# Optimization experiments

Hardware: AMD Instinct MI355X
Metric: run time of the kernel (lower is better)

## Reference

```python
import jax, jax.numpy as jnp
import numpy as np

N_HEAD = 16


def setup_inputs() -> dict:
    key = jax.random.key(0)
    ks = jax.random.split(key, 9)
    B, T, C = 4, 2048, 1024
    s = 1.0 / np.sqrt(C)
    x = jax.random.normal(ks[0], (B, T, C), dtype=jnp.float32)
    Wq = jax.random.normal(ks[1], (C, C), dtype=jnp.float32) * s
    bq = jax.random.normal(ks[2], (C,), dtype=jnp.float32) * 0.01
    Wk = jax.random.normal(ks[3], (C, C), dtype=jnp.float32) * s
    bk = jax.random.normal(ks[4], (C,), dtype=jnp.float32) * 0.01
    Wv = jax.random.normal(ks[5], (C, C), dtype=jnp.float32) * s
    bv = jax.random.normal(ks[6], (C,), dtype=jnp.float32) * 0.01
    Wp = jax.random.normal(ks[7], (C, C), dtype=jnp.float32) * s
    bp = jax.random.normal(ks[8], (C,), dtype=jnp.float32) * 0.01
    return {"x": x, "Wq": Wq, "bq": bq, "Wk": Wk, "bk": bk,
            "Wv": Wv, "bv": bv, "Wp": Wp, "bp": bp}


def reference(x, Wq, bq, Wk, bk, Wv, bv, Wp, bp):
    B, T, C = x.shape
    H = N_HEAD
    d = C // H
    # projections (torch Linear: x @ W.T + b)
    q = (x @ Wq.T + bq).reshape(B, T, H, d)  # [B,T,H,d]
    k = (x @ Wk.T + bk).reshape(B, T, H, d)
    v = (x @ Wv.T + bv).reshape(B, T, H, d)
    scale = 1.0 / jnp.sqrt(jnp.asarray(d, dtype=x.dtype))
    # scores: [B,H,T,T]
    att = jnp.einsum('bqhd,bkhd->bhqk', q, k) * scale
    causal = jnp.tril(jnp.ones((T, T), dtype=bool))  # [T,T]
    att = jnp.where(causal[None, None], att, jnp.asarray(-jnp.inf, dtype=att.dtype))
    att = jax.nn.softmax(att, axis=-1)
    y = jnp.einsum('bhqk,bkhd->bqhd', att, v).reshape(B, T, C)
    return y @ Wp.T + bp
```

## Files before the change

### kernel.cpp

```cpp
#include <hip/hip_runtime.h>
#include <hip/hip_bf16.h>

typedef __attribute__((ext_vector_type(8))) short bf16x8;
typedef __attribute__((ext_vector_type(4))) float f32x4;

static constexpr int Tt = 2048;
static constexpr int Cc = 1024;
static constexpr int Dd = 64;
static constexpr int Mm = 8192;

static constexpr size_t XN = (size_t)Mm * Cc;
static constexpr size_t WN = (size_t)Cc * Cc;

__device__ __forceinline__ void async_copy16(void* lds, const void* g) {
  __builtin_amdgcn_global_load_lds(
      (const __attribute__((address_space(1))) void*)g,
      (__attribute__((address_space(3))) void*)lds, 16, 0, 0);
}

__device__ __forceinline__ unsigned short f2bf(float f) {
  union { float f; unsigned int u; } v; v.f = f;
  unsigned int r = (v.u + 0x7fffu + ((v.u >> 16) & 1u)) >> 16;
  return (unsigned short)r;
}
__device__ __forceinline__ unsigned int pack2bf(float f0, float f1) {
  unsigned int b0 = __float_as_uint(f0) + 0x8000u;
  unsigned int b1 = __float_as_uint(f1) + 0x8000u;
  return (b1 & 0xffff0000u) | (b0 >> 16);
}
__device__ __forceinline__ unsigned int cvtpk2bf(float f0, float f1) {
  unsigned int r;
  asm("v_cvt_pk_bf16_f32 %0, %1, %2" : "=v"(r) : "v"(f0), "v"(f1));
  return r;
}
__device__ __forceinline__ uint4 ldconv_f32(const float* p) {
  float4 lo = *(const float4*)p;
  float4 hi = *(const float4*)(p + 4);
  uint4 r;
  r.x = pack2bf(lo.x, lo.y);
  r.y = pack2bf(lo.z, lo.w);
  r.z = pack2bf(hi.x, hi.y);
  r.w = pack2bf(hi.z, hi.w);
  return r;
}

__global__ __launch_bounds__(256) void convert_all(
    const float* __restrict__ x, const float* __restrict__ wq,
    const float* __restrict__ wk, const float* __restrict__ wv,
    unsigned short* __restrict__ dst,
    const float* __restrict__ wp, unsigned short* __restrict__ wpb)
{
  if (blockIdx.x >= 5632) {
    const size_t i = ((size_t)(blockIdx.x - 5632) * 256 + threadIdx.x) * 8;
    *(uint4*)(wpb + i) = ldconv_f32(wp + i);
    return;
  }
  const size_t i = ((size_t)blockIdx.x * 256 + threadIdx.x) * 8;
  const float* s; size_t off;
  if (i < XN)                { s = x;  off = 0; }
  else if (i < XN + WN)      { s = wq; off = XN; }
  else if (i < XN + 2 * WN)  { s = wk; off = XN + WN; }
  else                       { s = wv; off = XN + 2 * WN; }
  *(uint4*)(dst + i) = ldconv_f32(s + (i - off));
}

template <int MODE>
__device__ __forceinline__ void gemm_async_body(
    unsigned short* As, unsigned short* Bs,
    const unsigned short* __restrict__ A,
    const unsigned short* __restrict__ Bt,
    const float* __restrict__ bias,
    unsigned short* __restrict__ out, float mult)
{
  const int tid  = threadIdx.x;
  const int wave = tid >> 6;
  const int lane = tid & 63;
  const int m16  = lane & 15;
  const int quad = lane >> 4;
  const int row0 = blockIdx.x * 128;
  const int col0 = blockIdx.y * 128;
  const int wm = (wave >> 1) * 64;
  const int wn = (wave & 1) * 64;

  f32x4 acc[4][4] = {};

  const unsigned short* Ag[4];
  const unsigned short* Bg[4];
#pragma unroll
  for (int j = 0; j < 4; ++j) {
    const int c  = j * 256 + tid;
    const int rw = c >> 3;
    const int sw = (c & 7) ^ (rw & 7);
    Ag[j] = A  + (size_t)(row0 + rw) * Cc + sw * 8;
    Bg[j] = Bt + (size_t)(col0 + rw) * Cc + sw * 8;
  }

  for (int k0 = 0; k0 < Cc; k0 += 64) {
    __syncthreads();
#pragma unroll
    for (int j = 0; j < 4; ++j)
      async_copy16((char*)As + j * 4096 + wave * 1024, Ag[j] + k0);
#pragma unroll
    for (int j = 0; j < 4; ++j)
      async_copy16((char*)Bs + j * 4096 + wave * 1024, Bg[j] + k0);
    __syncthreads();
#pragma unroll
    for (int kk = 0; kk < 2; ++kk) {
      const int chp = (kk * 4 + quad) ^ (m16 & 7);
      bf16x8 af[4], bfr[4];
#pragma unroll
      for (int i = 0; i < 4; ++i)
        af[i] = *(const bf16x8*)(As + (wm + i * 16 + m16) * 64 + chp * 8);
#pragma unroll
      for (int j = 0; j < 4; ++j)
        bfr[j] = *(const bf16x8*)(Bs + (wn + j * 16 + m16) * 64 + chp * 8);
#pragma unroll
      for (int i = 0; i < 4; ++i)
#pragma unroll
        for (int j = 0; j < 4; ++j)
          acc[i][j] = __builtin_amdgcn_mfma_f32_16x16x32_bf16(af[i], bfr[j], acc[i][j], 0, 0, 0);
    }
  }

  float bvj[4];
#pragma unroll
  for (int j = 0; j < 4; ++j)
    bvj[j] = bias[col0 + wn + j * 16 + m16];
#pragma unroll
  for (int i = 0; i < 4; ++i) {
    const int rbase = row0 + wm + i * 16 + quad * 4;
#pragma unroll
    for (int j = 0; j < 4; ++j) {
      const int col = col0 + wn + j * 16 + m16;
      const float bv = bvj[j];
      if (MODE == 0) {
#pragma unroll
        for (int r = 0; r < 4; ++r)
          out[(size_t)(rbase + r) * Cc + col] = f2bf((acc[i][j][r] + bv) * mult);
      } else if (MODE == 1) {
        const int t0 = rbase & (Tt - 1);
        const int b  = rbase >> 11;
        ushort4 pk;
        pk.x = f2bf(acc[i][j][0] + bv);
        pk.y = f2bf(acc[i][j][1] + bv);
        pk.z = f2bf(acc[i][j][2] + bv);
        pk.w = f2bf(acc[i][j][3] + bv);
        *(ushort4*)(out + (size_t)(b * Cc + col) * Tt + t0) = pk;
      } else {
        float* outf = (float*)out;
#pragma unroll
        for (int r = 0; r < 4; ++r)
          outf[(size_t)(rbase + r) * Cc + col] = acc[i][j][r] + bv;
      }
    }
  }
}

__global__ __launch_bounds__(256) void qkv_gemm(
    const unsigned short* __restrict__ Xb,
    const unsigned short* __restrict__ Wqb, const float* __restrict__ bq,
    const unsigned short* __restrict__ Wkb, const float* __restrict__ bk,
    const unsigned short* __restrict__ Wvb, const float* __restrict__ bv,
    unsigned short* Qw, unsigned short* Kw, unsigned short* Vtw)
{
  __shared__ __align__(16) unsigned short smem[16384];
  const int z = blockIdx.z;
  if (z == 0)      gemm_async_body<0>(smem, smem + 8192, Xb, Wqb, bq, Qw, 0.125f * 1.44269504f);
  else if (z == 1) gemm_async_body<0>(smem, smem + 8192, Xb, Wkb, bk, Kw, 1.0f);
  else             gemm_async_body<1>(smem, smem + 8192, Xb, Wvb, bv, Vtw, 1.0f);
}

__global__ __launch_bounds__(256) void proj_gemm_pre(
    const unsigned short* __restrict__ Yb,
    const unsigned short* __restrict__ Wpb, const float* __restrict__ bp,
    float* __restrict__ out)
{
  __shared__ __align__(16) unsigned short smem[16384];
  gemm_async_body<2>(smem, smem + 8192, Yb, Wpb, bp, (unsigned short*)out, 1.0f);
}

__global__ __launch_bounds__(256) void attn_strip16(
    const unsigned short* __restrict__ Q,
    const unsigned short* __restrict__ Kg,
    const unsigned short* __restrict__ Vt,
    unsigned short* __restrict__ Y)
{
  __shared__ __align__(16) unsigned short KV[2 * 8192];

  const int tid  = threadIdx.x;
  const int wave = tid >> 6;
  const int lane = tid & 63;
  const int m16  = lane & 15;
  const int quad = lane >> 4;

  const int bh = blockIdx.x;
  const int p  = blockIdx.y;
  const int b = bh >> 4, h = bh & 15;

  const unsigned short* Kb = Kg + (size_t)(b * Tt) * Cc + h * Dd;
  const unsigned short* Vb = Vt + (size_t)(b * Cc + h * Dd) * Tt;

  const int maxH = 32 - p;
  const int TOT  = 33;
  const int chp  = quad ^ ((m16 >> 1) & 3);

  bf16x8 onesA;
#pragma unroll
  for (int i = 0; i < 8; ++i) onesA[i] = (short)0x3F80;

  const unsigned short* pK[2];
  const unsigned short* pV[2];
#pragma unroll
  for (int ii = 0; ii < 2; ++ii) {
    const int cc  = ii * 256 + tid;
    const int kkS = cc >> 8;
    const int rrS = (cc >> 2) & 63;
    const int chd = (cc & 3) ^ ((rrS >> 1) & 3);
    pK[ii] = Kb + (size_t)rrS * Cc + kkS * 32 + chd * 8;
    pV[ii] = Vb + (size_t)rrS * Tt + kkS * 32 + chd * 8;
  }
  const unsigned short* pK0[2] = {pK[0], pK[1]};
  const unsigned short* pV0[2] = {pV[0], pV[1]};

  int qw = (127 - 4 * p - wave) * 16;
  bf16x8 qf[2];
  {
    const unsigned short* Qb = Q + (size_t)(b * Tt + qw + m16) * Cc + h * Dd;
#pragma unroll
    for (int kk = 0; kk < 2; ++kk)
      qf[kk] = *(const bf16x8*)(Qb + kk * 32 + quad * 8);
  }
  f32x4 o[4] = {};
  f32x4 lz = {};

  auto writeout = [&](int qw_) {
    const float l = lz[0];
    const float inv = (l > 0.f) ? (1.0f / l) : 0.f;
    unsigned short* yp = Y + (size_t)(b * Tt + qw_ + m16) * Cc + h * Dd + quad * 4;
#pragma unroll
    for (int jn = 0; jn < 4; ++jn) {
      uint2 pk;
      pk.x = cvtpk2bf(o[jn][0] * inv, o[jn][1] * inv);
      pk.y = cvtpk2bf(o[jn][2] * inv, o[jn][3] * inv);
      *(uint2*)(yp + jn * 16) = pk;
    }
  };

  {
    char* KbufB = (char*)KV;
    char* VbufB = KbufB + 8192;
#pragma unroll
    for (int ii = 0; ii < 2; ++ii) {
      async_copy16(KbufB + ii * 4096 + wave * 1024, pK[ii]);
      async_copy16(VbufB + ii * 4096 + wave * 1024, pV[ii]);
    }
#pragma unroll
    for (int ii = 0; ii < 2; ++ii) { pK[ii] += 64 * Cc; pV[ii] += 64; }
  }

  for (int g = 0; g < TOT; ++g) {
    if (g == maxH) {
      writeout(qw);
      qw = (4 * p + wave) * 16;
      const unsigned short* Qb = Q + (size_t)(b * Tt + qw + m16) * Cc + h * Dd;
#pragma unroll
      for (int kk = 0; kk < 2; ++kk)
        qf[kk] = *(const bf16x8*)(Qb + kk * 32 + quad * 8);
#pragma unroll
      for (int jn = 0; jn < 4; ++jn)
        o[jn] = f32x4{0.f, 0.f, 0.f, 0.f};
      lz = f32x4{0.f, 0.f, 0.f, 0.f};
    }
    const int kt  = (g < maxH) ? g : g - maxH;
    const int k0  = kt * 64;
    const int buf = g & 1;

    __syncthreads();
    if (g + 1 < TOT) {
      if (g + 1 == maxH) {
#pragma unroll
        for (int ii = 0; ii < 2; ++ii) { pK[ii] = pK0[ii]; pV[ii] = pV0[ii]; }
      }
      char* KbufB = (char*)KV + (buf ^ 1) * 16384;
      char* VbufB = KbufB + 8192;
#pragma unroll
      for (int ii = 0; ii < 2; ++ii) {
        async_copy16(KbufB + ii * 4096 + wave * 1024, pK[ii]);
        async_copy16(VbufB + ii * 4096 + wave * 1024, pV[ii]);
      }
#pragma unroll
      for (int ii = 0; ii < 2; ++ii) { pK[ii] += 64 * Cc; pV[ii] += 64; }
    }

    const unsigned short* Kbuf = KV + buf * 8192;
    const unsigned short* Vbuf = Kbuf + 4096;
    bf16x8 kf[2][4], vf[2][4];
#pragma unroll
    for (int kk = 0; kk < 2; ++kk)
#pragma unroll
      for (int jn = 0; jn < 4; ++jn) {
        kf[kk][jn] = *(const bf16x8*)(Kbuf + kk * 2048 + (jn * 16 + m16) * 32 + chp * 8);
        vf[kk][jn] = *(const bf16x8*)(Vbuf + kk * 2048 + (jn * 16 + m16) * 32 + chp * 8);
      }

    const int smin = qw;
    f32x4 sv[4] = {};
    __builtin_amdgcn_s_setprio(1);
#pragma unroll
    for (int kk = 0; kk < 2; ++kk)
#pragma unroll
      for (int jn = 0; jn < 4; ++jn)
        sv[jn] = __builtin_amdgcn_mfma_f32_16x16x32_bf16(kf[kk][jn], qf[kk], sv[jn], 0, 0, 0);
    __builtin_amdgcn_s_setprio(0);

    if (k0 + 63 <= smin) {
#pragma unroll
      for (int jn = 0; jn < 4; ++jn)
#pragma unroll
        for (int r = 0; r < 4; ++r)
          sv[jn][r] = __builtin_exp2f(sv[jn][r]);
    } else {
      const int qcol = smin + m16;
#pragma unroll
      for (int jn = 0; jn < 4; ++jn)
#pragma unroll
        for (int r = 0; r < 4; ++r)
          sv[jn][r] = (k0 + jn * 16 + quad * 4 + r > qcol)
                          ? 0.f : __builtin_exp2f(sv[jn][r]);
    }

    unsigned int P2[4][2];
#pragma unroll
    for (int jn = 0; jn < 4; ++jn) {
      P2[jn][0] = cvtpk2bf(sv[jn][0], sv[jn][1]);
      P2[jn][1] = cvtpk2bf(sv[jn][2], sv[jn][3]);
    }
#pragma unroll
    for (int kk = 0; kk < 2; ++kk) {
      auto r0 = __builtin_amdgcn_permlane32_swap(P2[2 * kk][0], P2[2 * kk + 1][0], false, false);
      auto t0 = __builtin_amdgcn_permlane16_swap(r0[0], r0[1], false, false);
      auto r1 = __builtin_amdgcn_permlane32_swap(P2[2 * kk][1], P2[2 * kk + 1][1], false, false);
      auto t1 = __builtin_amdgcn_permlane16_swap(r1[0], r1[1], false, false);
      uint4 u;
      u.x = t0[0];
      u.y = t1[0];
      u.z = t0[1];
      u.w = t1[1];
      union { uint4 u4; bf16x8 bf; } cv; cv.u4 = u;
      __builtin_amdgcn_s_setprio(1);
      lz = __builtin_amdgcn_mfma_f32_16x16x32_bf16(onesA, cv.bf, lz, 0, 0, 0);
#pragma unroll
      for (int jn = 0; jn < 4; ++jn)
        o[jn] = __builtin_amdgcn_mfma_f32_16x16x32_bf16(vf[kk][jn], cv.bf, o[jn], 0, 0, 0);
      __builtin_amdgcn_s_setprio(0);
    }
  }

  writeout(qw);
}

__global__ __launch_bounds__(256) void proj_gemm(
    const unsigned short* __restrict__ Y,
    const float* __restrict__ Wp, const float* __restrict__ bp,
    float* __restrict__ out)
{
  __shared__ __align__(16) unsigned short As[8192];
  __shared__ __align__(16) unsigned short Bs[8192];
  const int tid  = threadIdx.x;
  const int wave = tid >> 6;
  const int lane = tid & 63;
  const int m16  = lane & 15;
  const int quad = lane >> 4;
  const int row0 = blockIdx.x * 128;
  const int col0 = blockIdx.y * 128;
  const int wm = (wave >> 1) * 64;
  const int wn = (wave & 1) * 64;
  const int chp = quad ^ ((m16 >> 1) & 3);

  f32x4 acc[4][4] = {};

  const int c0 = tid, c1 = 256 + tid;
  const int sw0 = (c0 & 3) ^ ((c0 >> 3) & 3);
  const int sw1 = (c1 & 3) ^ ((c1 >> 3) & 3);
  const unsigned short* Ag0 = Y + (size_t)(row0 + (c0 >> 2)) * Cc + sw0 * 8;
  const unsigned short* Ag1 = Y + (size_t)(row0 + (c1 >> 2)) * Cc + sw1 * 8;
  const float* Bg0 = Wp + (size_t)(col0 + (c0 >> 2)) * Cc + (c0 & 3) * 8;
  const float* Bg1 = Wp + (size_t)(col0 + (c1 >> 2)) * Cc + (c1 & 3) * 8;
  const int bd0 = ((c0 >> 2) * 4 + sw0) * 8;
  const int bd1 = ((c1 >> 2) * 4 + sw1) * 8;

  uint4 b0 = ldconv_f32(Bg0);
  uint4 b1 = ldconv_f32(Bg1);

  async_copy16((char*)As + wave * 1024,        Ag0);
  async_copy16((char*)As + 4096 + wave * 1024, Ag1);
  *(uint4*)(Bs + bd0) = b0;
  *(uint4*)(Bs + bd1) = b1;
  b0 = ldconv_f32(Bg0 + 32);
  b1 = ldconv_f32(Bg1 + 32);

  int buf = 0;
  for (int k0 = 0; k0 < Cc; k0 += 32) {
    __syncthreads();
    if (k0 + 32 < Cc) {
      char* Ab = (char*)As + (buf ^ 1) * 8192;
      async_copy16(Ab + wave * 1024,        Ag0 + k0 + 32);
      async_copy16(Ab + 4096 + wave * 1024, Ag1 + k0 + 32);
      *(uint4*)(Bs + (buf ^ 1) * 4096 + bd0) = b0;
      *(uint4*)(Bs + (buf ^ 1) * 4096 + bd1) = b1;
      if (k0 + 64 < Cc) {
        b0 = ldconv_f32(Bg0 + k0 + 64);
        b1 = ldconv_f32(Bg1 + k0 + 64);
      }
    }
    const unsigned short* Asb = As + buf * 4096;
    const unsigned short* Bsb = Bs + buf * 4096;
    bf16x8 af[4], bfr[4];
#pragma unroll
    for (int i = 0; i < 4; ++i)
      af[i] = *(const bf16x8*)(Asb + (wm + i * 16 + m16) * 32 + chp * 8);
#pragma unroll
    for (int j = 0; j < 4; ++j)
      bfr[j] = *(const bf16x8*)(Bsb + (wn + j * 16 + m16) * 32 + chp * 8);
#pragma unroll
    for (int i = 0; i < 4; ++i)
#pragma unroll
      for (int j = 0; j < 4; ++j)
        acc[i][j] = __builtin_amdgcn_mfma_f32_16x16x32_bf16(af[i], bfr[j], acc[i][j], 0, 0, 0);
    buf ^= 1;
  }

#pragma unroll
  for (int i = 0; i < 4; ++i) {
    const int rbase = row0 + wm + i * 16 + quad * 4;
#pragma unroll
    for (int j = 0; j < 4; ++j) {
      const int col = col0 + wn + j * 16 + m16;
      const float bv = bp[col];
#pragma unroll
      for (int r = 0; r < 4; ++r)
        out[(size_t)(rbase + r) * Cc + col] = acc[i][j][r] + bv;
    }
  }
}

extern "C" void kernel_launch(void* const* d_in, const int* in_sizes, int n_in,
                              void* d_out, int out_size, void* d_ws, size_t ws_size,
                              hipStream_t stream)
{
  const float* x  = (const float*)d_in[0];
  const float* Wq = (const float*)d_in[1];
  const float* bq = (const float*)d_in[2];
  const float* Wk = (const float*)d_in[3];
  const float* bk = (const float*)d_in[4];
  const float* Wv = (const float*)d_in[5];
  const float* bv = (const float*)d_in[6];
  const float* Wp = (const float*)d_in[7];
  const float* bp = (const float*)d_in[8];

  unsigned short* ws  = (unsigned short*)d_ws;
  unsigned short* Qw  = ws;
  unsigned short* Kw  = ws + (size_t)1 * XN;
  unsigned short* Vtw = ws + (size_t)2 * XN;
  unsigned short* Yw  = ws + (size_t)3 * XN;
  unsigned short* Wpb = ws + (size_t)4 * XN;
  const bool pre = ws_size >= ((size_t)4 * XN + WN) * sizeof(unsigned short);

  unsigned short* cvt = (unsigned short*)d_out;
  unsigned short* Xb  = cvt;
  unsigned short* Wqb = cvt + XN;
  unsigned short* Wkb = cvt + XN + WN;
  unsigned short* Wvb = cvt + XN + 2 * WN;
  float* out = (float*)d_out;

  convert_all<<<pre ? 6144 : 5632, 256, 0, stream>>>(x, Wq, Wk, Wv, cvt, Wp, Wpb);
  qkv_gemm<<<dim3(64, 8, 3), 256, 0, stream>>>(Xb, Wqb, bq, Wkb, bk, Wvb, bv, Qw, Kw, Vtw);
  attn_strip16<<<dim3(64, 16), 256, 0, stream>>>(Qw, Kw, Vtw, Yw);
  if (pre) proj_gemm_pre<<<dim3(64, 8), 256, 0, stream>>>(Yw, Wpb, bp, out);
  else     proj_gemm<<<dim3(64, 8), 256, 0, stream>>>(Yw, Wp, bp, out);
}
```

Baseline: 254.9 us.

## Fuse high and low query strips into one KV pass per block

The attention kernel now gives each wave four 16-row query strips: two from the high half and two from the low half. A single sweep over the KV tiles serves all four strips, and low strips skip tiles past their causal limit. Before, each wave handled one strip at a time and reloaded the K/V tiles for its second pass. Each staged K/V tile now feeds more MFMA work, and the grid is halved, which lowers parallelism and raises register use for the extra accumulators.

```diff
diff --git a/kernel.cpp b/kernel.cpp
--- a/kernel.cpp
+++ b/kernel.cpp
@@ -179,7 +179,7 @@
   gemm_async_body<2>(smem, smem + 8192, Yb, Wpb, bp, (unsigned short*)out, 1.0f);
 }
 
-__global__ __launch_bounds__(256) void attn_strip16(
+__global__ __launch_bounds__(256) void attn_fused(
     const unsigned short* __restrict__ Q,
     const unsigned short* __restrict__ Kg,
     const unsigned short* __restrict__ Vt,
@@ -200,9 +200,8 @@
   const unsigned short* Kb = Kg + (size_t)(b * Tt) * Cc + h * Dd;
   const unsigned short* Vb = Vt + (size_t)(b * Cc + h * Dd) * Tt;
 
-  const int maxH = 32 - p;
-  const int TOT  = 33;
-  const int chp  = quad ^ ((m16 >> 1) & 3);
+  const int TOT = 32 - 2 * p;
+  const int chp = quad ^ ((m16 >> 1) & 3);
 
   bf16x8 onesA;
 #pragma unroll
@@ -219,32 +218,21 @@
     pK[ii] = Kb + (size_t)rrS * Cc + kkS * 32 + chd * 8;
     pV[ii] = Vb + (size_t)rrS * Tt + kkS * 32 + chd * 8;
   }
-  const unsigned short* pK0[2] = {pK[0], pK[1]};
-  const unsigned short* pV0[2] = {pV[0], pV[1]};
-
-  int qw = (127 - 4 * p - wave) * 16;
-  bf16x8 qf[2];
-  {
-    const unsigned short* Qb = Q + (size_t)(b * Tt + qw + m16) * Cc + h * Dd;
+
+  const int qH = (63 - 4 * p - wave) * 32;
+  const int qL = (4 * p + wave) * 32;
+  int qrow[4] = {qH, qH + 16, qL, qL + 16};
+
+  bf16x8 qf[4][2];
+#pragma unroll
+  for (int u = 0; u < 4; ++u) {
+    const unsigned short* Qb = Q + (size_t)(b * Tt + qrow[u] + m16) * Cc + h * Dd;
 #pragma unroll
     for (int kk = 0; kk < 2; ++kk)
-      qf[kk] = *(const bf16x8*)(Qb + kk * 32 + quad * 8);
-  }
-  f32x4 o[4] = {};
-  f32x4 lz = {};
-
-  auto writeout = [&](int qw_) {
-    const float l = lz[0];
-    const float inv = (l > 0.f) ? (1.0f / l) : 0.f;
-    unsigned short* yp = Y + (size_t)(b * Tt + qw_ + m16) * Cc + h * Dd + quad * 4;
-#pragma unroll
-    for (int jn = 0; jn < 4; ++jn) {
-      uint2 pk;
-      pk.x = cvtpk2bf(o[jn][0] * inv, o[jn][1] * inv);
-      pk.y = cvtpk2bf(o[jn][2] * inv, o[jn][3] * inv);
-      *(uint2*)(yp + jn * 16) = pk;
-    }
-  };
+      qf[u][kk] = *(const bf16x8*)(Qb + kk * 32 + quad * 8);
+  }
+  f32x4 o[4][4] = {};
+  f32x4 lz[4] = {};
 
   {
     char* KbufB = (char*)KV;
@@ -259,28 +247,11 @@
   }
 
   for (int g = 0; g < TOT; ++g) {
-    if (g == maxH) {
-      writeout(qw);
-      qw = (4 * p + wave) * 16;
-      const unsigned short* Qb = Q + (size_t)(b * Tt + qw + m16) * Cc + h * Dd;
-#pragma unroll
-      for (int kk = 0; kk < 2; ++kk)
-        qf[kk] = *(const bf16x8*)(Qb + kk * 32 + quad * 8);
-#pragma unroll
-      for (int jn = 0; jn < 4; ++jn)
-        o[jn] = f32x4{0.f, 0.f, 0.f, 0.f};
-      lz = f32x4{0.f, 0.f, 0.f, 0.f};
-    }
-    const int kt  = (g < maxH) ? g : g - maxH;
-    const int k0  = kt * 64;
+    const int k0  = g * 64;
     const int buf = g & 1;
 
     __syncthreads();
     if (g + 1 < TOT) {
-      if (g + 1 == maxH) {
-#pragma unroll
-        for (int ii = 0; ii < 2; ++ii) { pK[ii] = pK0[ii]; pV[ii] = pV0[ii]; }
-      }
       char* KbufB = (char*)KV + (buf ^ 1) * 16384;
       char* VbufB = KbufB + 8192;
 #pragma unroll
@@ -303,60 +274,76 @@
         vf[kk][jn] = *(const bf16x8*)(Vbuf + kk * 2048 + (jn * 16 + m16) * 32 + chp * 8);
       }
 
-    const int smin = qw;
-    f32x4 sv[4] = {};
-    __builtin_amdgcn_s_setprio(1);
-#pragma unroll
-    for (int kk = 0; kk < 2; ++kk)
-#pragma unroll
-      for (int jn = 0; jn < 4; ++jn)
-        sv[jn] = __builtin_amdgcn_mfma_f32_16x16x32_bf16(kf[kk][jn], qf[kk], sv[jn], 0, 0, 0);
-    __builtin_amdgcn_s_setprio(0);
-
-    if (k0 + 63 <= smin) {
-#pragma unroll
-      for (int jn = 0; jn < 4; ++jn)
-#pragma unroll
-        for (int r = 0; r < 4; ++r)
-          sv[jn][r] = __builtin_exp2f(sv[jn][r]);
-    } else {
-      const int qcol = smin + m16;
-#pragma unroll
-      for (int jn = 0; jn < 4; ++jn)
-#pragma unroll
-        for (int r = 0; r < 4; ++r)
-          sv[jn][r] = (k0 + jn * 16 + quad * 4 + r > qcol)
-                          ? 0.f : __builtin_exp2f(sv[jn][r]);
-    }
-
-    unsigned int P2[4][2];
+#pragma unroll
+    for (int u = 0; u < 4; ++u) {
+      const int smin = qrow[u];
+      if (k0 > smin + 15) continue;
+      f32x4 sv[4] = {};
+      __builtin_amdgcn_s_setprio(1);
+#pragma unroll
+      for (int kk = 0; kk < 2; ++kk)
+#pragma unroll
+        for (int jn = 0; jn < 4; ++jn)
+          sv[jn] = __builtin_amdgcn_mfma_f32_16x16x32_bf16(kf[kk][jn], qf[u][kk], sv[jn], 0, 0, 0);
+      __builtin_amdgcn_s_setprio(0);
+
+      if (k0 + 63 <= smin) {
+#pragma unroll
+        for (int jn = 0; jn < 4; ++jn)
+#pragma unroll
+          for (int r = 0; r < 4; ++r)
+            sv[jn][r] = __builtin_exp2f(sv[jn][r]);
+      } else {
+        const int qcol = smin + m16;
+#pragma unroll
+        for (int jn = 0; jn < 4; ++jn)
+#pragma unroll
+          for (int r = 0; r < 4; ++r)
+            sv[jn][r] = (k0 + jn * 16 + quad * 4 + r > qcol)
+                            ? 0.f : __builtin_exp2f(sv[jn][r]);
+      }
+
+      unsigned int P2[4][2];
+#pragma unroll
+      for (int jn = 0; jn < 4; ++jn) {
+        P2[jn][0] = cvtpk2bf(sv[jn][0], sv[jn][1]);
+        P2[jn][1] = cvtpk2bf(sv[jn][2], sv[jn][3]);
+      }
+#pragma unroll
+      for (int kk = 0; kk < 2; ++kk) {
+        auto r0 = __builtin_amdgcn_permlane32_swap(P2[2 * kk][0], P2[2 * kk + 1][0], false, false);
+        auto t0 = __builtin_amdgcn_permlane16_swap(r0[0], r0[1], false, false);
+        auto r1 = __builtin_amdgcn_permlane32_swap(P2[2 * kk][1], P2[2 * kk + 1][1], false, false);
+        auto t1 = __builtin_amdgcn_permlane16_swap(r1[0], r1[1], false, false);
+        uint4 u4;
+        u4.x = t0[0];
+        u4.y = t1[0];
+        u4.z = t0[1];
+        u4.w = t1[1];
+        union { uint4 uu; bf16x8 bf; } cv; cv.uu = u4;
+        __builtin_amdgcn_s_setprio(1);
+        lz[u] = __builtin_amdgcn_mfma_f32_16x16x32_bf16(onesA, cv.bf, lz[u], 0, 0, 0);
+#pragma unroll
+        for (int jn = 0; jn < 4; ++jn)
+          o[u][jn] = __builtin_amdgcn_mfma_f32_16x16x32_bf16(vf[kk][jn], cv.bf, o[u][jn], 0, 0, 0);
+        __builtin_amdgcn_s_setprio(0);
+      }
+    }
+  }
+
+#pragma unroll
+  for (int u = 0; u < 4; ++u) {
+    const float l = lz[u][0];
+    const float inv = (l > 0.f) ? (1.0f / l) : 0.f;
+    unsigned short* yp = Y + (size_t)(b * Tt + qrow[u] + m16) * Cc + h * Dd + quad * 4;
 #pragma unroll
     for (int jn = 0; jn < 4; ++jn) {
-      P2[jn][0] = cvtpk2bf(sv[jn][0], sv[jn][1]);
-      P2[jn][1] = cvtpk2bf(sv[jn][2], sv[jn][3]);
-    }
-#pragma unroll
-    for (int kk = 0; kk < 2; ++kk) {
-      auto r0 = __builtin_amdgcn_permlane32_swap(P2[2 * kk][0], P2[2 * kk + 1][0], false, false);
-      auto t0 = __builtin_amdgcn_permlane16_swap(r0[0], r0[1], false, false);
-      auto r1 = __builtin_amdgcn_permlane32_swap(P2[2 * kk][1], P2[2 * kk + 1][1], false, false);
-      auto t1 = __builtin_amdgcn_permlane16_swap(r1[0], r1[1], false, false);
-      uint4 u;
-      u.x = t0[0];
-      u.y = t1[0];
-      u.z = t0[1];
-      u.w = t1[1];
-      union { uint4 u4; bf16x8 bf; } cv; cv.u4 = u;
-      __builtin_amdgcn_s_setprio(1);
-      lz = __builtin_amdgcn_mfma_f32_16x16x32_bf16(onesA, cv.bf, lz, 0, 0, 0);
-#pragma unroll
-      for (int jn = 0; jn < 4; ++jn)
-        o[jn] = __builtin_amdgcn_mfma_f32_16x16x32_bf16(vf[kk][jn], cv.bf, o[jn], 0, 0, 0);
-      __builtin_amdgcn_s_setprio(0);
-    }
-  }
-
-  writeout(qw);
+      uint2 pk;
+      pk.x = cvtpk2bf(o[u][jn][0] * inv, o[u][jn][1] * inv);
+      pk.y = cvtpk2bf(o[u][jn][2] * inv, o[u][jn][3] * inv);
+      *(uint2*)(yp + jn * 16) = pk;
+    }
+  }
 }
 
 __global__ __launch_bounds__(256) void proj_gemm(
@@ -475,7 +462,7 @@
 
   convert_all<<<pre ? 6144 : 5632, 256, 0, stream>>>(x, Wq, Wk, Wv, cvt, Wp, Wpb);
   qkv_gemm<<<dim3(64, 8, 3), 256, 0, stream>>>(Xb, Wqb, bq, Wkb, bk, Wvb, bv, Qw, Kw, Vtw);
-  attn_strip16<<<dim3(64, 16), 256, 0, stream>>>(Qw, Kw, Vtw, Yw);
+  attn_fused<<<dim3(64, 8), 256, 0, stream>>>(Qw, Kw, Vtw, Yw);
   if (pre) proj_gemm_pre<<<dim3(64, 8), 256, 0, stream>>>(Yw, Wpb, bp, out);
   else     proj_gemm<<<dim3(64, 8), 256, 0, stream>>>(Yw, Wp, bp, out);
 }
```

New measurement: 287.2 us. 12.7% more time.
